# Performance work log

Hardware: AMD Instinct MI355X
Metric: run time of the kernel (lower is better)

The kernel has to match this reference:

```python
import jax, jax.numpy as jnp
import numpy as np

IN, H, OUT, B = 1024, 4096, 1, 4096


def setup_inputs() -> dict:
    key = jax.random.key(0)
    ks = jax.random.split(key, 20)
    sx = 1.0 / np.sqrt(IN)
    sh = 1.0 / np.sqrt(H)
    d = {
        "x": jax.random.normal(ks[0], (B, IN), jnp.float32),
        "hidden": jax.random.normal(ks[1], (B, H), jnp.float32),
        "cell": jax.random.normal(ks[2], (B, H), jnp.float32),
        # input projections (Linear(input_size, h_size)), weight [H, IN], bias [H]
        "Wx_i": jax.random.normal(ks[3], (H, IN), jnp.float32) * sx,
        "Wx_f": jax.random.normal(ks[4], (H, IN), jnp.float32) * sx,
        "Wx_o": jax.random.normal(ks[5], (H, IN), jnp.float32) * sx,
        "Wx_c": jax.random.normal(ks[6], (H, IN), jnp.float32) * sx,
        "bx_i": jax.random.normal(ks[7], (H,), jnp.float32) * sx,
        "bx_f": jax.random.normal(ks[8], (H,), jnp.float32) * sx,
        "bx_o": jax.random.normal(ks[9], (H,), jnp.float32) * sx,
        "bx_c": jax.random.normal(ks[10], (H,), jnp.float32) * sx,
        # hidden projections (Linear(h_size, h_size, bias=False)), weight [H, H]
        "Wh_i": jax.random.normal(ks[11], (H, H), jnp.float32) * sh,
        "Wh_f": jax.random.normal(ks[12], (H, H), jnp.float32) * sh,
        "Wh_o": jax.random.normal(ks[13], (H, H), jnp.float32) * sh,
        "Wh_c": jax.random.normal(ks[14], (H, H), jnp.float32) * sh,
        # output head Linear(h_size, out_size)
        "Wy": jax.random.normal(ks[15], (OUT, H), jnp.float32) * sh,
        "by": jax.random.normal(ks[16], (OUT,), jnp.float32) * sh,
    }
    return d


def reference(x, hidden, cell,
              Wx_i, Wx_f, Wx_o, Wx_c,
              bx_i, bx_f, bx_o, bx_c,
              Wh_i, Wh_f, Wh_o, Wh_c,
              Wy, by):
    # single LSTM step, batched over leading dim
    i = jax.nn.sigmoid(x @ Wx_i.T + bx_i + hidden @ Wh_i.T)
    f = jax.nn.sigmoid(x @ Wx_f.T + bx_f + hidden @ Wh_f.T)
    o = jax.nn.sigmoid(x @ Wx_o.T + bx_o + hidden @ Wh_o.T)
    c_til = jnp.tanh(x @ Wx_c.T + bx_c + hidden @ Wh_c.T)
    c_new = f * cell + i * c_til
    h_new = o * jnp.tanh(c_new)
    y_hat = h_new @ Wy.T + by  # [B, OUT]
    return y_hat
```

## Files before the change

### kernel.cpp

```cpp
#include <hip/hip_runtime.h>
#include <stdint.h>

#define IN_ 1024
#define H_  4096
#define B_  4096
#define K_  5120
#define NT_ 80

typedef short bf16x8 __attribute__((ext_vector_type(8)));
typedef float f32x4  __attribute__((ext_vector_type(4)));

__device__ __forceinline__ unsigned short f2bf(float x) {
    union { float f; uint32_t u; } v; v.f = x;
    return (unsigned short)((v.u + 0x7FFFu + ((v.u >> 16) & 1u)) >> 16);
}
__device__ __forceinline__ float bf2f(uint32_t u16) {
    union { uint32_t u; float f; } v; v.u = u16 << 16; return v.f;
}

__global__ __launch_bounds__(256) void cvt_cat(
    const float* __restrict__ s1, const float* __restrict__ s2,
    unsigned short* __restrict__ dst)
{
    int idx = blockIdx.x * 256 + threadIdx.x;
    int r = idx / (K_ / 4);
    int c = (idx % (K_ / 4)) * 4;
    float4 v;
    if (c < IN_) v = *(const float4*)(s1 + (size_t)r * IN_ + c);
    else         v = *(const float4*)(s2 + (size_t)r * H_ + (c - IN_));
    ushort4 o = { f2bf(v.x), f2bf(v.y), f2bf(v.z), f2bf(v.w) };
    *(ushort4*)(dst + (size_t)r * K_ + c) = o;
}

__device__ __forceinline__ int swz(int row) { return ((row >> 1) & 3) << 4; }

__global__ __launch_bounds__(512, 2) void gemm_gate8(
    const unsigned short* __restrict__ A,
    const unsigned short* __restrict__ W,
    const float* __restrict__ bias,
    unsigned short* __restrict__ P)
{
    __shared__ __align__(16) char ldsb[131072];

    const int tid  = threadIdx.x;
    const int wid  = tid >> 6;
    const int lane = tid & 63;

    const int wg = (blockIdx.x & 7) * 32 + (blockIdx.x >> 3);
    const int mt = wg & 15, nt = wg >> 4;
    const int bm = mt * 256, bn = nt * 256;

    const int wm = wid >> 2;
    const int wn = wid & 3;

    const int l15 = lane & 15;
    const int c0  = (lane >> 4) << 4;

    const int q0  = wid * 64 + lane;
    const int r0  = q0 >> 2;
    const int cb0 = ((q0 & 3) << 4) ^ swz(r0);
    const int r1  = r0 + 128;
    const int cb1 = ((q0 & 3) << 4) ^ swz(r1);

    f32x4 acc[8][4];
#pragma unroll
    for (int i = 0; i < 8; ++i)
#pragma unroll
        for (int j = 0; j < 4; ++j) acc[i][j] = (f32x4){0.f, 0.f, 0.f, 0.f};

    auto stage = [&](int isB, int ksel, int tau) {
        if (tau >= NT_) tau = NT_ - 2 + (tau & 1);
        const int kbase = tau * 64 + ksel * 32;
        const int chunk = (tau & 1) * 65536 + isB * 32768 + ksel * 16384;
        const unsigned short* src = isB ? W : A;
        const int gb = isB ? bn : bm;
        __builtin_amdgcn_global_load_lds(
            (const __attribute__((address_space(1))) void*)(src + (size_t)(gb + r0) * K_ + kbase + (cb0 >> 1)),
            (__attribute__((address_space(3))) void*)(ldsb + chunk + wid * 1024), 16, 0, 0);
        __builtin_amdgcn_global_load_lds(
            (const __attribute__((address_space(1))) void*)(src + (size_t)(gb + r1) * K_ + kbase + (cb1 >> 1)),
            (__attribute__((address_space(3))) void*)(ldsb + chunk + 8192 + wid * 1024), 16, 0, 0);
    };

    stage(0, 0, 0); stage(0, 1, 0); stage(1, 0, 0); stage(1, 1, 0);
    stage(1, 0, 1); stage(1, 1, 1);
    asm volatile("s_waitcnt vmcnt(4)" ::: "memory");
    __builtin_amdgcn_s_barrier();

    for (int i = 0; i < NT_ / 2; ++i) {
        const int T0 = 2 * i;
        bf16x8 b[2][4];
#pragma unroll
        for (int k = 0; k < 8; ++k) {
            const int half = k >> 2;
            const int q    = k & 3;
            const char* Abase = ldsb + half * 65536;
            const char* Bbase = Abase + 32768;

            bf16x8 a0[2], a1[2];
            if (q == 0) {
#pragma unroll
                for (int ni = 0; ni < 4; ++ni) {
                    const int row = wn * 64 + ni * 16 + l15;
                    b[0][ni] = *(const bf16x8*)(Bbase + row * 64 + (c0 ^ swz(row)));
                }
            }
#pragma unroll
            for (int mi = 0; mi < 2; ++mi) {
                const int row = wm * 128 + q * 32 + mi * 16 + l15;
                a0[mi] = *(const bf16x8*)(Abase + row * 64 + (c0 ^ swz(row)));
            }
            if (q == 0) {
#pragma unroll
                for (int ni = 0; ni < 4; ++ni) {
                    const int row = wn * 64 + ni * 16 + l15;
                    b[1][ni] = *(const bf16x8*)(Bbase + 16384 + row * 64 + (c0 ^ swz(row)));
                }
            }
#pragma unroll
            for (int mi = 0; mi < 2; ++mi) {
                const int row = wm * 128 + q * 32 + mi * 16 + l15;
                a1[mi] = *(const bf16x8*)(Abase + 16384 + row * 64 + (c0 ^ swz(row)));
            }

            if (q == 3) asm volatile("s_waitcnt vmcnt(2)" ::: "memory");
            __builtin_amdgcn_s_barrier();

            if      (k == 0) stage(0, 0, T0 + 1);
            else if (k == 1) stage(0, 1, T0 + 1);
            else if (k == 2) stage(1, 0, T0 + 2);
            else if (k == 3) stage(1, 1, T0 + 2);
            else if (k == 4) stage(0, 0, T0 + 2);
            else if (k == 5) stage(0, 1, T0 + 2);
            else if (k == 6) stage(1, 0, T0 + 3);
            else             stage(1, 1, T0 + 3);
            __builtin_amdgcn_sched_barrier(0);

            __builtin_amdgcn_s_setprio(1);
#pragma unroll
            for (int mi = 0; mi < 2; ++mi)
#pragma unroll
                for (int ni = 0; ni < 4; ++ni)
                    acc[q * 2 + mi][ni] = __builtin_amdgcn_mfma_f32_16x16x32_bf16(
                        a0[mi], b[0][ni], acc[q * 2 + mi][ni], 0, 0, 0);
#pragma unroll
            for (int mi = 0; mi < 2; ++mi)
#pragma unroll
                for (int ni = 0; ni < 4; ++ni)
                    acc[q * 2 + mi][ni] = __builtin_amdgcn_mfma_f32_16x16x32_bf16(
                        a1[mi], b[1][ni], acc[q * 2 + mi][ni], 0, 0, 0);
            __builtin_amdgcn_s_setprio(0);
        }
    }

    asm volatile("s_waitcnt vmcnt(0)" ::: "memory");
    __builtin_amdgcn_s_barrier();

#pragma unroll
    for (int ni = 0; ni < 4; ++ni) {
        const int col = wn * 64 + ni * 16 + l15;
        const float bv = bias[bn + col];
#pragma unroll
        for (int mi = 0; mi < 8; ++mi) {
            const int rowb = wm * 128 + mi * 16 + (lane >> 4) * 4;
#pragma unroll
            for (int r = 0; r < 4; ++r) {
                const int row  = rowb + r;
                const int byte = row * 512 + ((col * 2) ^ ((row & 7) << 4));
                *(unsigned short*)(ldsb + byte) = f2bf(acc[mi][ni][r] + bv);
            }
        }
    }
    __builtin_amdgcn_s_barrier();

#pragma unroll
    for (int c = 0; c < 16; ++c) {
        const int idx = c * 512 + tid;
        const int row = idx >> 5;
        const int cb  = (idx & 31) * 16;
        bf16x8 v = *(const bf16x8*)(ldsb + row * 512 + (cb ^ ((row & 7) << 4)));
        *(bf16x8*)&P[(size_t)(bm + row) * H_ + bn + cb / 2] = v;
    }
}

__global__ __launch_bounds__(256) void gates_gemv(
    const unsigned short* __restrict__ Pi, const unsigned short* __restrict__ Pf,
    const unsigned short* __restrict__ Po, const unsigned short* __restrict__ Pc,
    const float* __restrict__ cell, const float* __restrict__ Wy,
    const float* __restrict__ by, float* __restrict__ y)
{
    const int b = blockIdx.x;
    const int t = threadIdx.x;
    const size_t base = (size_t)b * H_;
    float part = 0.f;

#pragma unroll
    for (int j = 0; j < 4; ++j) {
        const int h = j * 1024 + t * 4;
        const uint2 ri = *(const uint2*)(Pi + base + h);
        const uint2 rf = *(const uint2*)(Pf + base + h);
        const uint2 ro = *(const uint2*)(Po + base + h);
        const uint2 rc = *(const uint2*)(Pc + base + h);
        const float4 cv = *(const float4*)(cell + base + h);
        const float4 wv = *(const float4*)(Wy + h);

        const uint32_t zi[4] = { ri.x & 0xffffu, ri.x >> 16, ri.y & 0xffffu, ri.y >> 16 };
        const uint32_t zf[4] = { rf.x & 0xffffu, rf.x >> 16, rf.y & 0xffffu, rf.y >> 16 };
        const uint32_t zo[4] = { ro.x & 0xffffu, ro.x >> 16, ro.y & 0xffffu, ro.y >> 16 };
        const uint32_t zc[4] = { rc.x & 0xffffu, rc.x >> 16, rc.y & 0xffffu, rc.y >> 16 };
        const float cc[4] = { cv.x, cv.y, cv.z, cv.w };
        const float ww[4] = { wv.x, wv.y, wv.z, wv.w };
#pragma unroll
        for (int e = 0; e < 4; ++e) {
            const float ig = 1.f / (1.f + __expf(-bf2f(zi[e])));
            const float fg = 1.f / (1.f + __expf(-bf2f(zf[e])));
            const float og = 1.f / (1.f + __expf(-bf2f(zo[e])));
            const float ct = tanhf(bf2f(zc[e]));
            const float cn = fg * cc[e] + ig * ct;
            const float hn = og * tanhf(cn);
            part += hn * ww[e];
        }
    }

#pragma unroll
    for (int off = 32; off > 0; off >>= 1) part += __shfl_down(part, off, 64);
    __shared__ float red[4];
    if ((t & 63) == 0) red[t >> 6] = part;
    __syncthreads();
    if (t == 0) y[b] = red[0] + red[1] + red[2] + red[3] + by[0];
}

extern "C" void kernel_launch(void* const* d_in, const int* in_sizes, int n_in,
                              void* d_out, int out_size, void* d_ws, size_t ws_size,
                              hipStream_t stream) {
    const float* x      = (const float*)d_in[0];
    const float* hidden = (const float*)d_in[1];
    const float* cell   = (const float*)d_in[2];
    const float* Wx[4]  = { (const float*)d_in[3], (const float*)d_in[4],
                            (const float*)d_in[5], (const float*)d_in[6] };
    const float* bx[4]  = { (const float*)d_in[7], (const float*)d_in[8],
                            (const float*)d_in[9], (const float*)d_in[10] };
    const float* Wh[4]  = { (const float*)d_in[11], (const float*)d_in[12],
                            (const float*)d_in[13], (const float*)d_in[14] };
    const float* Wy     = (const float*)d_in[15];
    const float* by     = (const float*)d_in[16];
    float* y = (float*)d_out;

    unsigned short* Ab = (unsigned short*)d_ws;
    unsigned short* Wb = Ab + (size_t)B_ * K_;
    unsigned short* Pg[4];
    {
        unsigned short* p0 = Wb + (size_t)H_ * K_;
        for (int g = 0; g < 4; ++g) Pg[g] = p0 + (size_t)g * B_ * H_;
    }

    const int cvt_grid = (B_ * (K_ / 4)) / 256;
    cvt_cat<<<cvt_grid, 256, 0, stream>>>(x, hidden, Ab);

    for (int g = 0; g < 4; ++g) {
        cvt_cat<<<cvt_grid, 256, 0, stream>>>(Wx[g], Wh[g], Wb);
        gemm_gate8<<<256, 512, 0, stream>>>(Ab, Wb, bx[g], Pg[g]);
    }

    gates_gemv<<<B_, 256, 0, stream>>>(Pg[0], Pg[1], Pg[2], Pg[3], cell, Wy, by, y);
}
```

Measured before the change: 676.5 us.

## Overlap next gate's weight conversion with current gate GEMM via extra blocks

Appends 256 extra blocks to each gate GEMM launch (except the last); they convert the next gate's fp32 weights to bf16 into a second, double-buffered workspace. Three of the four standalone weight-conversion launches now overlap with GEMM compute instead of running serially. In exchange, the GEMM kernel needs 128 KB of LDS per block and the extra conversion blocks compete with GEMM tiles for CUs and bandwidth. The path also needs a larger workspace, with a fallback to the old schedule when the workspace is too small.

```diff
diff --git a/kernel.cpp b/kernel.cpp
--- a/kernel.cpp
+++ b/kernel.cpp
@@ -38,8 +38,27 @@
     const unsigned short* __restrict__ A,
     const unsigned short* __restrict__ W,
     const float* __restrict__ bias,
-    unsigned short* __restrict__ P)
+    unsigned short* __restrict__ P,
+    const float* __restrict__ cWx,
+    const float* __restrict__ cWh,
+    unsigned short* __restrict__ cDst)
 {
+    if (blockIdx.x >= 256) {
+        const int base = (int)(blockIdx.x - 256) * 512 + (int)threadIdx.x;
+#pragma unroll 4
+        for (int j = 0; j < 40; ++j) {
+            const int idx = j * 131072 + base;
+            const int r = idx / (K_ / 4);
+            const int c = (idx % (K_ / 4)) * 4;
+            float4 v;
+            if (c < IN_) v = *(const float4*)(cWx + (size_t)r * IN_ + c);
+            else         v = *(const float4*)(cWh + (size_t)r * H_ + (c - IN_));
+            ushort4 o = { f2bf(v.x), f2bf(v.y), f2bf(v.z), f2bf(v.w) };
+            *(ushort4*)(cDst + (size_t)r * K_ + c) = o;
+        }
+        return;
+    }
+
     __shared__ __align__(16) char ldsb[131072];
 
     const int tid  = threadIdx.x;
@@ -246,21 +265,44 @@
     const float* by     = (const float*)d_in[16];
     float* y = (float*)d_out;
 
-    unsigned short* Ab = (unsigned short*)d_ws;
-    unsigned short* Wb = Ab + (size_t)B_ * K_;
-    unsigned short* Pg[4];
-    {
-        unsigned short* p0 = Wb + (size_t)H_ * K_;
-        for (int g = 0; g < 4; ++g) Pg[g] = p0 + (size_t)g * B_ * H_;
-    }
-
     const int cvt_grid = (B_ * (K_ / 4)) / 256;
-    cvt_cat<<<cvt_grid, 256, 0, stream>>>(x, hidden, Ab);
-
-    for (int g = 0; g < 4; ++g) {
-        cvt_cat<<<cvt_grid, 256, 0, stream>>>(Wx[g], Wh[g], Wb);
-        gemm_gate8<<<256, 512, 0, stream>>>(Ab, Wb, bx[g], Pg[g]);
-    }
-
-    gates_gemv<<<B_, 256, 0, stream>>>(Pg[0], Pg[1], Pg[2], Pg[3], cell, Wy, by, y);
-}
+    const size_t WKE = (size_t)H_ * K_;
+
+    if (ws_size >= (size_t)260046848) {
+        unsigned short* Ab  = (unsigned short*)d_ws;
+        unsigned short* Wb0 = Ab  + WKE;
+        unsigned short* Wb1 = Wb0 + WKE;
+        unsigned short* Pg[4];
+        for (int g = 0; g < 4; ++g) Pg[g] = Wb1 + WKE + (size_t)g * B_ * H_;
+        unsigned short* Wbuf[2] = { Wb0, Wb1 };
+
+        cvt_cat<<<cvt_grid, 256, 0, stream>>>(x, hidden, Ab);
+        cvt_cat<<<cvt_grid, 256, 0, stream>>>(Wx[0], Wh[0], Wb0);
+        for (int g = 0; g < 4; ++g) {
+            if (g < 3)
+                gemm_gate8<<<512, 512, 0, stream>>>(Ab, Wbuf[g & 1], bx[g], Pg[g],
+                                                    Wx[g + 1], Wh[g + 1], Wbuf[(g + 1) & 1]);
+            else
+                gemm_gate8<<<256, 512, 0, stream>>>(Ab, Wbuf[g & 1], bx[g], Pg[g],
+                                                    (const float*)nullptr,
+                                                    (const float*)nullptr,
+                                                    (unsigned short*)nullptr);
+        }
+        gates_gemv<<<B_, 256, 0, stream>>>(Pg[0], Pg[1], Pg[2], Pg[3], cell, Wy, by, y);
+    } else {
+        unsigned short* Ab = (unsigned short*)d_ws;
+        unsigned short* Wb = Ab + WKE;
+        unsigned short* Pg[4];
+        for (int g = 0; g < 4; ++g) Pg[g] = Wb + WKE + (size_t)g * B_ * H_;
+
+        cvt_cat<<<cvt_grid, 256, 0, stream>>>(x, hidden, Ab);
+        for (int g = 0; g < 4; ++g) {
+            cvt_cat<<<cvt_grid, 256, 0, stream>>>(Wx[g], Wh[g], Wb);
+            gemm_gate8<<<256, 512, 0, stream>>>(Ab, Wb, bx[g], Pg[g],
+                                                (const float*)nullptr,
+                                                (const float*)nullptr,
+                                                (unsigned short*)nullptr);
+        }
+        gates_gemv<<<B_, 256, 0, stream>>>(Pg[0], Pg[1], Pg[2], Pg[3], cell, Wy, by, y);
+    }
+}
```

After: 693.2 us. 2.5% more time.

## Batch weight conversions and four gate GEMMs into single launches

Applied to the files above, without the earlier changes.

Converts activations and all four gate weight matrices to bf16 in one launch, and runs all four gate GEMMs in one 1024-block grid, selecting the gate by block index. This removes serialisation between per-gate conversion and GEMM, and fills the GPU better than 256-block launches. It needs a much larger workspace holding all four converted weights, and falls back to the old sequential path when the workspace is too small.

```diff
diff --git a/kernel.cpp b/kernel.cpp
--- a/kernel.cpp
+++ b/kernel.cpp
@@ -18,11 +18,20 @@
     union { uint32_t u; float f; } v; v.u = u16 << 16; return v.f;
 }
 
-__global__ __launch_bounds__(256) void cvt_cat(
-    const float* __restrict__ s1, const float* __restrict__ s2,
-    unsigned short* __restrict__ dst)
+__global__ __launch_bounds__(256) void cvt_cat5(
+    const float* __restrict__ a1, const float* __restrict__ a2, unsigned short* __restrict__ ad,
+    const float* __restrict__ b1, const float* __restrict__ b2, unsigned short* __restrict__ bd,
+    const float* __restrict__ c1, const float* __restrict__ c2, unsigned short* __restrict__ cd,
+    const float* __restrict__ d1, const float* __restrict__ d2, unsigned short* __restrict__ dd,
+    const float* __restrict__ e1, const float* __restrict__ e2, unsigned short* __restrict__ ed)
 {
-    int idx = blockIdx.x * 256 + threadIdx.x;
+    const int unit = blockIdx.x / 20480;
+    const int sub  = blockIdx.x - unit * 20480;
+    const float* s1 = (unit == 0) ? a1 : (unit == 1) ? b1 : (unit == 2) ? c1 : (unit == 3) ? d1 : e1;
+    const float* s2 = (unit == 0) ? a2 : (unit == 1) ? b2 : (unit == 2) ? c2 : (unit == 3) ? d2 : e2;
+    unsigned short* dst = (unit == 0) ? ad : (unit == 1) ? bd : (unit == 2) ? cd : (unit == 3) ? dd : ed;
+
+    int idx = sub * 256 + threadIdx.x;
     int r = idx / (K_ / 4);
     int c = (idx % (K_ / 4)) * 4;
     float4 v;
@@ -36,17 +45,26 @@
 
 __global__ __launch_bounds__(512, 2) void gemm_gate8(
     const unsigned short* __restrict__ A,
-    const unsigned short* __restrict__ W,
-    const float* __restrict__ bias,
-    unsigned short* __restrict__ P)
+    const unsigned short* __restrict__ W0, const unsigned short* __restrict__ W1,
+    const unsigned short* __restrict__ W2, const unsigned short* __restrict__ W3,
+    const float* __restrict__ bias0, const float* __restrict__ bias1,
+    const float* __restrict__ bias2, const float* __restrict__ bias3,
+    unsigned short* __restrict__ P0, unsigned short* __restrict__ P1,
+    unsigned short* __restrict__ P2, unsigned short* __restrict__ P3)
 {
+    const int gate = blockIdx.x >> 8;
+    const unsigned short* W = (gate == 0) ? W0 : (gate == 1) ? W1 : (gate == 2) ? W2 : W3;
+    const float* bias = (gate == 0) ? bias0 : (gate == 1) ? bias1 : (gate == 2) ? bias2 : bias3;
+    unsigned short* P = (gate == 0) ? P0 : (gate == 1) ? P1 : (gate == 2) ? P2 : P3;
+
     __shared__ __align__(16) char ldsb[131072];
 
     const int tid  = threadIdx.x;
     const int wid  = tid >> 6;
     const int lane = tid & 63;
 
-    const int wg = (blockIdx.x & 7) * 32 + (blockIdx.x >> 3);
+    const int b8 = blockIdx.x & 255;
+    const int wg = (b8 & 7) * 32 + (b8 >> 3);
     const int mt = wg & 15, nt = wg >> 4;
     const int bm = mt * 256, bn = nt * 256;
 
@@ -246,21 +264,49 @@
     const float* by     = (const float*)d_in[16];
     float* y = (float*)d_out;
 
-    unsigned short* Ab = (unsigned short*)d_ws;
-    unsigned short* Wb = Ab + (size_t)B_ * K_;
-    unsigned short* Pg[4];
-    {
-        unsigned short* p0 = Wb + (size_t)H_ * K_;
-        for (int g = 0; g < 4; ++g) Pg[g] = p0 + (size_t)g * B_ * H_;
-    }
-
     const int cvt_grid = (B_ * (K_ / 4)) / 256;
-    cvt_cat<<<cvt_grid, 256, 0, stream>>>(x, hidden, Ab);
-
-    for (int g = 0; g < 4; ++g) {
-        cvt_cat<<<cvt_grid, 256, 0, stream>>>(Wx[g], Wh[g], Wb);
-        gemm_gate8<<<256, 512, 0, stream>>>(Ab, Wb, bx[g], Pg[g]);
-    }
-
-    gates_gemv<<<B_, 256, 0, stream>>>(Pg[0], Pg[1], Pg[2], Pg[3], cell, Wy, by, y);
-}
+    const size_t WKE = (size_t)H_ * K_;
+    const size_t PKE = (size_t)B_ * H_;
+    const size_t need = (WKE * 5 + PKE * 4) * sizeof(unsigned short);
+
+    if (ws_size >= need) {
+        unsigned short* Ab = (unsigned short*)d_ws;
+        unsigned short* Wb[4];
+        for (int g = 0; g < 4; ++g) Wb[g] = Ab + WKE * (1 + g);
+        unsigned short* Pg[4];
+        for (int g = 0; g < 4; ++g) Pg[g] = Ab + WKE * 5 + (size_t)g * PKE;
+
+        cvt_cat5<<<5 * cvt_grid, 256, 0, stream>>>(
+            x, hidden, Ab,
+            Wx[0], Wh[0], Wb[0], Wx[1], Wh[1], Wb[1],
+            Wx[2], Wh[2], Wb[2], Wx[3], Wh[3], Wb[3]);
+
+        gemm_gate8<<<1024, 512, 0, stream>>>(
+            Ab, Wb[0], Wb[1], Wb[2], Wb[3],
+            bx[0], bx[1], bx[2], bx[3],
+            Pg[0], Pg[1], Pg[2], Pg[3]);
+
+        gates_gemv<<<B_, 256, 0, stream>>>(Pg[0], Pg[1], Pg[2], Pg[3], cell, Wy, by, y);
+    } else {
+        unsigned short* Ab = (unsigned short*)d_ws;
+        unsigned short* Wb = Ab + WKE;
+        unsigned short* Pg[4];
+        for (int g = 0; g < 4; ++g) Pg[g] = Wb + WKE + (size_t)g * PKE;
+
+        cvt_cat5<<<cvt_grid, 256, 0, stream>>>(
+            x, hidden, Ab,
+            nullptr, nullptr, nullptr, nullptr, nullptr, nullptr,
+            nullptr, nullptr, nullptr, nullptr, nullptr, nullptr);
+        for (int g = 0; g < 4; ++g) {
+            cvt_cat5<<<cvt_grid, 256, 0, stream>>>(
+                Wx[g], Wh[g], Wb,
+                nullptr, nullptr, nullptr, nullptr, nullptr, nullptr,
+                nullptr, nullptr, nullptr, nullptr, nullptr, nullptr);
+            gemm_gate8<<<256, 512, 0, stream>>>(
+                Ab, Wb, Wb, Wb, Wb,
+                bx[g], bx[g], bx[g], bx[g],
+                Pg[g], Pg[g], Pg[g], Pg[g]);
+        }
+        gates_gemv<<<B_, 256, 0, stream>>>(Pg[0], Pg[1], Pg[2], Pg[3], cell, Wy, by, y);
+    }
+}
```

Result: slower. 726.2 us (+7.4%).
